# Performance work log

Measured on AMD Instinct MI355X. Metric: run time of the kernel, lower is better.

The kernel has to match this reference:

```python
import jax, jax.numpy as jnp
import numpy as np

N_NODES = 50000
N_EDGES = 800000
NODE_IN = 64
EDGE_IN = 64
MSG = 64
NODE_OUT = 64
EDGE_OUT = 64
DIM = 2


def setup_inputs() -> dict:
    key = jax.random.key(0)
    ks = jax.random.split(key, 12)
    x = jax.random.normal(ks[0], (N_NODES, NODE_IN), dtype=jnp.float32)
    edge_index = jax.random.randint(ks[1], (2, N_EDGES), 0, N_NODES, dtype=jnp.int64)
    edge_attr = jax.random.normal(ks[2], (N_EDGES, EDGE_IN), dtype=jnp.float32)
    r = jax.random.normal(ks[3], (N_EDGES, DIM), dtype=jnp.float32)
    # reference distances must be positive (divided by in strain computation)
    d_init = jax.random.uniform(ks[4], (N_EDGES, 1), dtype=jnp.float32, minval=0.5, maxval=1.5)
    msg_in = 1 + 2 * NODE_IN + EDGE_IN  # strain(1) + x_j + x_i + edge_attr
    W_msg = jax.random.normal(ks[5], (msg_in, MSG), dtype=jnp.float32) / np.sqrt(msg_in)
    b_msg = jnp.zeros((MSG,), dtype=jnp.float32)
    upd_in = NODE_IN + MSG
    W_upd = jax.random.normal(ks[6], (upd_in, NODE_OUT), dtype=jnp.float32) / np.sqrt(upd_in)
    b_upd = jnp.zeros((NODE_OUT,), dtype=jnp.float32)
    W_edge = jax.random.normal(ks[7], (MSG, EDGE_OUT), dtype=jnp.float32) / np.sqrt(MSG)
    b_edge = jnp.zeros((EDGE_OUT,), dtype=jnp.float32)
    return {"x": x, "edge_index": edge_index, "edge_attr": edge_attr, "r": r,
            "d_init": d_init, "W_msg": W_msg, "b_msg": b_msg, "W_upd": W_upd,
            "b_upd": b_upd, "W_edge": W_edge, "b_edge": b_edge}


def reference(x, edge_index, edge_attr, r, d_init, W_msg, b_msg, W_upd, b_upd, W_edge, b_edge):
    # PyG source_to_target flow: x_j = source = edge_index[0], x_i = target = edge_index[1]
    src = edge_index[0]
    dst = edge_index[1]
    n = x.shape[0]
    d = jnp.linalg.norm(r, axis=-1, keepdims=True)          # [e,1]
    strain = (d - d_init) / d_init                          # [e,1]
    # message: Linear(concat(x_j, x_i, strain, edge_attr)) -> Softplus
    feat = jnp.concatenate([x[src], x[dst], strain, edge_attr], axis=1)  # [e, 1+2*node_in+edge_in]
    msg = jax.nn.softplus(feat @ W_msg + b_msg)             # [e, msg]
    # mean aggregation over incoming edges per target node
    agg = jax.ops.segment_sum(msg, dst, num_segments=n)     # [n, msg]
    cnt = jax.ops.segment_sum(jnp.ones((msg.shape[0], 1), msg.dtype), dst, num_segments=n)
    agg = agg / jnp.maximum(cnt, 1.0)
    # node update: Linear(concat(x, aggr_out))
    x_new = jnp.concatenate([x, agg], axis=1) @ W_upd + b_upd  # [n, node_out]
    # edge update: Linear(messages)
    edge_new = msg @ W_edge + b_edge                        # [e, edge_out]
    return (x_new, edge_new, msg, strain)
```

## Files before the change

kernel.cpp:

```cpp
#include <hip/hip_runtime.h>
#include <math.h>

#define NN 50000
#define NE 800000
#define NTILE2 6250
#define NBLK 196

typedef __bf16 bf16x4 __attribute__((ext_vector_type(4)));
typedef __bf16 bf16x8 __attribute__((ext_vector_type(8)));
typedef float  f32x4  __attribute__((ext_vector_type(4)));

__device__ __forceinline__ float softplus_f(float v) {
    const float t = __expf(-fabsf(v));
    return fmaxf(v, 0.f) + __logf(1.f + t);
}

__global__ void k_prep(const float* __restrict__ x, __bf16* __restrict__ xb) {
    const int i = blockIdx.x * 256 + threadIdx.x;
    if (i < NN * 16) {
        const f32x4 v = *(const f32x4*)(x + (size_t)i * 4);
        bf16x4 b;
        b[0]=(__bf16)v[0]; b[1]=(__bf16)v[1]; b[2]=(__bf16)v[2]; b[3]=(__bf16)v[3];
        *(bf16x4*)(xb + (size_t)i * 4) = b;
    }
}

__global__ void k_zero(int* deg) {
    int i = blockIdx.x * blockDim.x + threadIdx.x;
    if (i < NN) deg[i] = 0;
}

__global__ void k_hist(const int* __restrict__ ei, int* __restrict__ deg) {
    int e = blockIdx.x * blockDim.x + threadIdx.x;
    if (e < NE) atomicAdd(&deg[ei[NE + e]], 1);
}

__global__ void k_bsum(const int* __restrict__ deg, int* __restrict__ bsum) {
    __shared__ int ws4[4];
    const int tid = threadIdx.x;
    const int i = blockIdx.x * 256 + tid;
    int v = (i < NN) ? deg[i] : 0;
    #pragma unroll
    for (int off = 1; off < 64; off <<= 1) v += __shfl_xor(v, off);
    if ((tid & 63) == 0) ws4[tid >> 6] = v;
    __syncthreads();
    if (tid == 0) bsum[blockIdx.x] = ws4[0] + ws4[1] + ws4[2] + ws4[3];
}

__global__ void k_bscan(const int* __restrict__ bsum, int* __restrict__ boff) {
    __shared__ int wsum[4];
    const int tid = threadIdx.x, lane = tid & 63, wid = tid >> 6;
    const int v = (tid < NBLK) ? bsum[tid] : 0;
    int s = v;
    #pragma unroll
    for (int off = 1; off < 64; off <<= 1) {
        int t = __shfl_up(s, off);
        if (lane >= off) s += t;
    }
    if (lane == 63) wsum[wid] = s;
    __syncthreads();
    int add = 0;
    #pragma unroll
    for (int q = 0; q < 4; ++q) add += (q < wid) ? wsum[q] : 0;
    if (tid < NBLK) boff[tid] = (s + add) - v;
}

__global__ void k_apply(const int* __restrict__ deg, const int* __restrict__ boff,
                        int* __restrict__ rowptr, int* __restrict__ cursor) {
    __shared__ int wsum[4];
    const int tid = threadIdx.x, lane = tid & 63, wid = tid >> 6;
    const int i = blockIdx.x * 256 + tid;
    const int v = (i < NN) ? deg[i] : 0;
    int s = v;
    #pragma unroll
    for (int off = 1; off < 64; off <<= 1) {
        int t = __shfl_up(s, off);
        if (lane >= off) s += t;
    }
    if (lane == 63) wsum[wid] = s;
    __syncthreads();
    int add = boff[blockIdx.x];
    #pragma unroll
    for (int q = 0; q < 4; ++q) add += (q < wid) ? wsum[q] : 0;
    const int incl = s + add;
    if (i < NN) { rowptr[i + 1] = incl; cursor[i] = incl - v; }
    if (i == 0) rowptr[0] = 0;
}

__global__ void k_scatter(const int* __restrict__ ei, int* __restrict__ cursor,
                          int* __restrict__ eidx) {
    int e = blockIdx.x * blockDim.x + threadIdx.x;
    if (e < NE) {
        int d = ei[NE + e];
        int p = atomicAdd(&cursor[d], 1);
        eidx[p] = e;
    }
}

template<bool USE_XB>
__global__ __launch_bounds__(512, 2) void k_edge(
    const float* __restrict__ x, const __bf16* __restrict__ xb,
    const int* __restrict__ ei,
    const float* __restrict__ ea, const float* __restrict__ r2,
    const float* __restrict__ dinit, const float* __restrict__ Wmsg,
    const float* __restrict__ bmsg, const float* __restrict__ Wedge,
    const float* __restrict__ bedge,
    float* __restrict__ out_edge, float* __restrict__ out_msg,
    float* __restrict__ out_strain)
{
    __shared__ __bf16 sWm[64 * 200];
    __shared__ __bf16 sA [128 * 200];
    __shared__ float  sStrain[128];

    const int tid  = threadIdx.x;
    const int lane = tid & 63;
    const int wid  = tid >> 6;
    const int col  = lane & 15;
    const int quad = lane >> 4;

    {
        const int n = tid & 63, kg = tid >> 6;
        for (int k = kg; k < 192; k += 8) {
            float v = (k < 128) ? Wmsg[k * 64 + n] : Wmsg[(k + 1) * 64 + n];
            sWm[n * 200 + k] = (__bf16)v;
        }
    }
    bf16x8 weF[2][4];
    #pragma unroll
    for (int kc = 0; kc < 2; ++kc)
        #pragma unroll
        for (int nt = 0; nt < 4; ++nt) {
            bf16x8 f;
            #pragma unroll
            for (int j = 0; j < 8; ++j)
                f[j] = (__bf16)Wedge[(kc * 32 + quad * 8 + j) * 64 + nt * 16 + col];
            weF[kc][nt] = f;
        }
    float bm[4], be[4], wst[4];
    #pragma unroll
    for (int nt = 0; nt < 4; ++nt) {
        bm[nt]  = bmsg[nt * 16 + col];
        be[nt]  = bedge[nt * 16 + col];
        wst[nt] = Wmsg[128 * 64 + nt * 16 + col];
    }

    for (int tile = blockIdx.x; tile < NTILE2; tile += gridDim.x) {
        const int e0 = tile * 128;

        if constexpr (USE_XB) {
            #pragma unroll
            for (int it = 0; it < 2; ++it) {
                const int i = tid + it * 512;
                const int e = i >> 3, c = i & 7;
                const int s = ei[e0 + e], d = ei[NE + e0 + e];
                const bf16x8 vj = *(const bf16x8*)(xb + (size_t)s * 64 + c * 8);
                const bf16x8 vi = *(const bf16x8*)(xb + (size_t)d * 64 + c * 8);
                *(bf16x8*)&sA[e * 200 +      c * 8] = vj;
                *(bf16x8*)&sA[e * 200 + 64 + c * 8] = vi;
            }
        } else {
            #pragma unroll
            for (int it = 0; it < 4; ++it) {
                const int i = tid + it * 512;
                const int e = i >> 4, c = i & 15;
                const int s = ei[e0 + e], d = ei[NE + e0 + e];
                const f32x4 xj = *(const f32x4*)(x + (size_t)s * 64 + c * 4);
                const f32x4 xi = *(const f32x4*)(x + (size_t)d * 64 + c * 4);
                bf16x4 a, b;
                a[0]=(__bf16)xj[0]; a[1]=(__bf16)xj[1]; a[2]=(__bf16)xj[2]; a[3]=(__bf16)xj[3];
                b[0]=(__bf16)xi[0]; b[1]=(__bf16)xi[1]; b[2]=(__bf16)xi[2]; b[3]=(__bf16)xi[3];
                *(bf16x4*)&sA[e * 200 +      c * 4] = a;
                *(bf16x4*)&sA[e * 200 + 64 + c * 4] = b;
            }
        }
        #pragma unroll
        for (int it = 0; it < 4; ++it) {
            const int i = tid + it * 512;
            const int e = i >> 4, c = i & 15;
            const f32x4 ev = __builtin_nontemporal_load(
                                 (const f32x4*)(ea + (size_t)(e0 + e) * 64 + c * 4));
            bf16x4 d;
            d[0]=(__bf16)ev[0]; d[1]=(__bf16)ev[1]; d[2]=(__bf16)ev[2]; d[3]=(__bf16)ev[3];
            *(bf16x4*)&sA[e * 200 + 128 + c * 4] = d;
        }
        if (tid < 128) {
            const float rx = r2[(size_t)(e0 + tid) * 2];
            const float ry = r2[(size_t)(e0 + tid) * 2 + 1];
            const float di = dinit[e0 + tid];
            const float st = (sqrtf(rx * rx + ry * ry) - di) / di;
            sStrain[tid] = st;
            __builtin_nontemporal_store(st, &out_strain[e0 + tid]);
        }
        __syncthreads();

        f32x4 acc[4];
        const int r0 = wid * 16 + quad * 4;
        #pragma unroll
        for (int nt = 0; nt < 4; ++nt)
            #pragma unroll
            for (int rg = 0; rg < 4; ++rg)
                acc[nt][rg] = sStrain[r0 + rg] * wst[nt];

        const int abase = (wid * 16 + col) * 200 + quad * 8;
        #pragma unroll
        for (int kc = 0; kc < 6; ++kc) {
            const bf16x8 af = *(const bf16x8*)&sA[abase + kc * 32];
            #pragma unroll
            for (int nt = 0; nt < 4; ++nt) {
                const bf16x8 bfr = *(const bf16x8*)&sWm[(nt * 16 + col) * 200 + kc * 32 + quad * 8];
                acc[nt] = __builtin_amdgcn_mfma_f32_16x16x32_bf16(af, bfr, acc[nt], 0, 0, 0);
            }
        }

        __bf16* A2 = &sA[wid * 16 * 200];
        #pragma unroll
        for (int nt = 0; nt < 4; ++nt) {
            #pragma unroll
            for (int rg = 0; rg < 4; ++rg) {
                const int row = quad * 4 + rg;
                const float sp = softplus_f(acc[nt][rg] + bm[nt]);
                out_msg[(size_t)(e0 + wid * 16 + row) * 64 + nt * 16 + col] = sp;
                A2[row * 88 + nt * 16 + col] = (__bf16)sp;
            }
        }
        __builtin_amdgcn_sched_barrier(0);

        f32x4 acc2[4];
        #pragma unroll
        for (int nt = 0; nt < 4; ++nt) acc2[nt] = (f32x4){0.f, 0.f, 0.f, 0.f};
        #pragma unroll
        for (int kc = 0; kc < 2; ++kc) {
            const bf16x8 af = *(const bf16x8*)&A2[col * 88 + kc * 32 + quad * 8];
            #pragma unroll
            for (int nt = 0; nt < 4; ++nt)
                acc2[nt] = __builtin_amdgcn_mfma_f32_16x16x32_bf16(af, weF[kc][nt], acc2[nt], 0, 0, 0);
        }
        #pragma unroll
        for (int nt = 0; nt < 4; ++nt) {
            #pragma unroll
            for (int rg = 0; rg < 4; ++rg) {
                __builtin_nontemporal_store(
                    acc2[nt][rg] + be[nt],
                    &out_edge[(size_t)(e0 + wid * 16 + quad * 4 + rg) * 64 + nt * 16 + col]);
            }
        }
        __syncthreads();
    }
}

__global__ __launch_bounds__(256) void k_node(
    const float* __restrict__ x, const float* __restrict__ msg,
    const int* __restrict__ rowptr, const int* __restrict__ eidx,
    const float* __restrict__ Wupd, const float* __restrict__ bupd,
    float* __restrict__ out_x)
{
    __shared__ float sW[128 * 64];
    const int tid = threadIdx.x;
    for (int i = tid; i < 2048; i += 256)
        ((f32x4*)sW)[i] = ((const f32x4*)Wupd)[i];
    __syncthreads();

    const int lane = tid & 63, wid = tid >> 6;
    const float bu = bupd[lane];

    for (int n = blockIdx.x * 4 + wid; n < NN; n += gridDim.x * 4) {
        const int rs = rowptr[n], ren = rowptr[n + 1];

        float a0 = 0.f, a1 = 0.f, a2 = 0.f, a3 = 0.f;
        int j = rs;
        for (; j + 4 <= ren; j += 4) {
            const int e0 = eidx[j], e1 = eidx[j + 1], e2 = eidx[j + 2], e3 = eidx[j + 3];
            a0 += msg[(size_t)e0 * 64 + lane];
            a1 += msg[(size_t)e1 * 64 + lane];
            a2 += msg[(size_t)e2 * 64 + lane];
            a3 += msg[(size_t)e3 * 64 + lane];
        }
        for (; j < ren; ++j) a0 += msg[(size_t)eidx[j] * 64 + lane];
        const float acc  = (a0 + a1) + (a2 + a3);
        const float mean = acc / fmaxf((float)(ren - rs), 1.f);
        const float xr   = x[(size_t)n * 64 + lane];

        float o = bu;
        #pragma unroll 16
        for (int k = 0; k < 64; ++k)
            o += __shfl(xr, k) * sW[k * 64 + lane];
        #pragma unroll 16
        for (int k = 0; k < 64; ++k)
            o += __shfl(mean, k) * sW[(64 + k) * 64 + lane];

        out_x[(size_t)n * 64 + lane] = o;
    }
}

extern "C" void kernel_launch(void* const* d_in, const int* in_sizes, int n_in,
                              void* d_out, int out_size, void* d_ws, size_t ws_size,
                              hipStream_t stream) {
    const float* x     = (const float*)d_in[0];
    const int*   ei    = (const int*)d_in[1];
    const float* ea    = (const float*)d_in[2];
    const float* r2    = (const float*)d_in[3];
    const float* dinit = (const float*)d_in[4];
    const float* Wmsg  = (const float*)d_in[5];
    const float* bmsg  = (const float*)d_in[6];
    const float* Wupd  = (const float*)d_in[7];
    const float* bupd  = (const float*)d_in[8];
    const float* Wedge = (const float*)d_in[9];
    const float* bedge = (const float*)d_in[10];

    float* out_x      = (float*)d_out;
    float* out_edge   = out_x + (size_t)NN * 64;
    float* out_msg    = out_edge + (size_t)NE * 64;
    float* out_strain = out_msg + (size_t)NE * 64;

    const size_t XB_BYTES  = (size_t)NN * 64 * 2;
    const size_t CSR_INTS  = 50176 + 50304 + 50176 + 800000 + 256 + 256;
    const bool   use_xb    = ws_size >= XB_BYTES + CSR_INTS * 4 + 64;

    __bf16* xb  = (__bf16*)d_ws;
    int*    deg = use_xb ? (int*)((char*)d_ws + XB_BYTES) : (int*)d_ws;
    int* rowptr = deg + 50176;
    int* cursor = rowptr + 50304;
    int* eidx   = cursor + 50176;
    int* bsum   = eidx + 800000;
    int* boff   = bsum + 256;

    k_zero   <<<196,   256, 0, stream>>>(deg);
    k_hist   <<<3125,  256, 0, stream>>>(ei, deg);
    k_bsum   <<<196,   256, 0, stream>>>(deg, bsum);
    k_bscan  <<<1,     256, 0, stream>>>(bsum, boff);
    k_apply  <<<196,   256, 0, stream>>>(deg, boff, rowptr, cursor);
    k_scatter<<<3125,  256, 0, stream>>>(ei, cursor, eidx);
    if (use_xb) {
        k_prep        <<<3125, 256, 0, stream>>>(x, xb);
        k_edge<true>  <<<512,  512, 0, stream>>>(x, xb, ei, ea, r2, dinit, Wmsg, bmsg,
                                                 Wedge, bedge, out_edge, out_msg, out_strain);
    } else {
        k_edge<false> <<<512,  512, 0, stream>>>(x, nullptr, ei, ea, r2, dinit, Wmsg, bmsg,
                                                 Wedge, bedge, out_edge, out_msg, out_strain);
    }
    k_node   <<<2048,  256, 0, stream>>>(x, out_msg, rowptr, eidx, Wupd, bupd, out_x);
}
```

Before: 797.8 us.

## Fuse mean aggregation into edge kernel via float atomics, drop CSR build

When the workspace is large enough, the edge kernel adds each softplus message into a per-node aggregation buffer with float atomics. This replaces the CSR construction (block sums, scan, apply, scatter) and the node kernel's gather that re-read all messages. The node kernel now reads the summed buffer and divides by the degree histogram. The cost is tens of millions of global atomics contending on destination rows, and summation order is no longer deterministic; the old CSR path remains as a fallback.

```diff
diff --git a/kernel.cpp b/kernel.cpp
--- a/kernel.cpp
+++ b/kernel.cpp
@@ -15,7 +15,8 @@
     return fmaxf(v, 0.f) + __logf(1.f + t);
 }
 
-__global__ void k_prep(const float* __restrict__ x, __bf16* __restrict__ xb) {
+__global__ void k_init(const float* __restrict__ x, __bf16* __restrict__ xb,
+                       int* __restrict__ deg, float* __restrict__ agg) {
     const int i = blockIdx.x * 256 + threadIdx.x;
     if (i < NN * 16) {
         const f32x4 v = *(const f32x4*)(x + (size_t)i * 4);
@@ -23,16 +24,190 @@
         b[0]=(__bf16)v[0]; b[1]=(__bf16)v[1]; b[2]=(__bf16)v[2]; b[3]=(__bf16)v[3];
         *(bf16x4*)(xb + (size_t)i * 4) = b;
     }
+    *(f32x4*)(agg + (size_t)i * 4) = (f32x4){0.f, 0.f, 0.f, 0.f};
+    if (i < NN) deg[i] = 0;
+}
+
+__global__ void k_hist(const int* __restrict__ ei, int* __restrict__ deg) {
+    int e = blockIdx.x * blockDim.x + threadIdx.x;
+    if (e < NE) atomicAdd(&deg[ei[NE + e]], 1);
+}
+
+__global__ __launch_bounds__(512, 2) void k_edge_agg(
+    const __bf16* __restrict__ xb, const int* __restrict__ ei,
+    const float* __restrict__ ea, const float* __restrict__ r2,
+    const float* __restrict__ dinit, const float* __restrict__ Wmsg,
+    const float* __restrict__ bmsg, const float* __restrict__ Wedge,
+    const float* __restrict__ bedge,
+    float* __restrict__ out_edge, float* __restrict__ out_msg,
+    float* __restrict__ out_strain, float* __restrict__ agg)
+{
+    __shared__ __bf16 sWm[64 * 200];
+    __shared__ __bf16 sA [128 * 200];
+    __shared__ float  sStrain[128];
+
+    const int tid  = threadIdx.x;
+    const int lane = tid & 63;
+    const int wid  = tid >> 6;
+    const int col  = lane & 15;
+    const int quad = lane >> 4;
+
+    {
+        const int n = tid & 63, kg = tid >> 6;
+        for (int k = kg; k < 192; k += 8) {
+            float v = (k < 128) ? Wmsg[k * 64 + n] : Wmsg[(k + 1) * 64 + n];
+            sWm[n * 200 + k] = (__bf16)v;
+        }
+    }
+    bf16x8 weF[2][4];
+    #pragma unroll
+    for (int kc = 0; kc < 2; ++kc)
+        #pragma unroll
+        for (int nt = 0; nt < 4; ++nt) {
+            bf16x8 f;
+            #pragma unroll
+            for (int j = 0; j < 8; ++j)
+                f[j] = (__bf16)Wedge[(kc * 32 + quad * 8 + j) * 64 + nt * 16 + col];
+            weF[kc][nt] = f;
+        }
+    float bm[4], be[4], wst[4];
+    #pragma unroll
+    for (int nt = 0; nt < 4; ++nt) {
+        bm[nt]  = bmsg[nt * 16 + col];
+        be[nt]  = bedge[nt * 16 + col];
+        wst[nt] = Wmsg[128 * 64 + nt * 16 + col];
+    }
+
+    for (int tile = blockIdx.x; tile < NTILE2; tile += gridDim.x) {
+        const int e0 = tile * 128;
+
+        #pragma unroll
+        for (int it = 0; it < 2; ++it) {
+            const int i = tid + it * 512;
+            const int e = i >> 3, c = i & 7;
+            const int s = ei[e0 + e], d = ei[NE + e0 + e];
+            const bf16x8 vj = *(const bf16x8*)(xb + (size_t)s * 64 + c * 8);
+            const bf16x8 vi = *(const bf16x8*)(xb + (size_t)d * 64 + c * 8);
+            *(bf16x8*)&sA[e * 200 +      c * 8] = vj;
+            *(bf16x8*)&sA[e * 200 + 64 + c * 8] = vi;
+        }
+        #pragma unroll
+        for (int it = 0; it < 4; ++it) {
+            const int i = tid + it * 512;
+            const int e = i >> 4, c = i & 15;
+            const f32x4 ev = __builtin_nontemporal_load(
+                                 (const f32x4*)(ea + (size_t)(e0 + e) * 64 + c * 4));
+            bf16x4 d;
+            d[0]=(__bf16)ev[0]; d[1]=(__bf16)ev[1]; d[2]=(__bf16)ev[2]; d[3]=(__bf16)ev[3];
+            *(bf16x4*)&sA[e * 200 + 128 + c * 4] = d;
+        }
+        if (tid < 128) {
+            const float rx = r2[(size_t)(e0 + tid) * 2];
+            const float ry = r2[(size_t)(e0 + tid) * 2 + 1];
+            const float di = dinit[e0 + tid];
+            const float st = (sqrtf(rx * rx + ry * ry) - di) / di;
+            sStrain[tid] = st;
+            __builtin_nontemporal_store(st, &out_strain[e0 + tid]);
+        }
+        __syncthreads();
+
+        f32x4 acc[4];
+        const int r0 = wid * 16 + quad * 4;
+        #pragma unroll
+        for (int nt = 0; nt < 4; ++nt)
+            #pragma unroll
+            for (int rg = 0; rg < 4; ++rg)
+                acc[nt][rg] = sStrain[r0 + rg] * wst[nt];
+
+        const int abase = (wid * 16 + col) * 200 + quad * 8;
+        #pragma unroll
+        for (int kc = 0; kc < 6; ++kc) {
+            const bf16x8 af = *(const bf16x8*)&sA[abase + kc * 32];
+            #pragma unroll
+            for (int nt = 0; nt < 4; ++nt) {
+                const bf16x8 bfr = *(const bf16x8*)&sWm[(nt * 16 + col) * 200 + kc * 32 + quad * 8];
+                acc[nt] = __builtin_amdgcn_mfma_f32_16x16x32_bf16(af, bfr, acc[nt], 0, 0, 0);
+            }
+        }
+
+        int dstv[4];
+        #pragma unroll
+        for (int rg = 0; rg < 4; ++rg)
+            dstv[rg] = ei[NE + e0 + r0 + rg];
+
+        __bf16* A2 = &sA[wid * 16 * 200];
+        #pragma unroll
+        for (int nt = 0; nt < 4; ++nt) {
+            #pragma unroll
+            for (int rg = 0; rg < 4; ++rg) {
+                const int row = quad * 4 + rg;
+                const float sp = softplus_f(acc[nt][rg] + bm[nt]);
+                __builtin_nontemporal_store(
+                    sp, &out_msg[(size_t)(e0 + wid * 16 + row) * 64 + nt * 16 + col]);
+                unsafeAtomicAdd(&agg[(size_t)dstv[rg] * 64 + nt * 16 + col], sp);
+                A2[row * 88 + nt * 16 + col] = (__bf16)sp;
+            }
+        }
+        __builtin_amdgcn_sched_barrier(0);
+
+        f32x4 acc2[4];
+        #pragma unroll
+        for (int nt = 0; nt < 4; ++nt) acc2[nt] = (f32x4){0.f, 0.f, 0.f, 0.f};
+        #pragma unroll
+        for (int kc = 0; kc < 2; ++kc) {
+            const bf16x8 af = *(const bf16x8*)&A2[col * 88 + kc * 32 + quad * 8];
+            #pragma unroll
+            for (int nt = 0; nt < 4; ++nt)
+                acc2[nt] = __builtin_amdgcn_mfma_f32_16x16x32_bf16(af, weF[kc][nt], acc2[nt], 0, 0, 0);
+        }
+        #pragma unroll
+        for (int nt = 0; nt < 4; ++nt) {
+            #pragma unroll
+            for (int rg = 0; rg < 4; ++rg) {
+                __builtin_nontemporal_store(
+                    acc2[nt][rg] + be[nt],
+                    &out_edge[(size_t)(e0 + wid * 16 + quad * 4 + rg) * 64 + nt * 16 + col]);
+            }
+        }
+        __syncthreads();
+    }
+}
+
+__global__ __launch_bounds__(256) void k_node_lite(
+    const float* __restrict__ x, const float* __restrict__ agg,
+    const int* __restrict__ deg,
+    const float* __restrict__ Wupd, const float* __restrict__ bupd,
+    float* __restrict__ out_x)
+{
+    __shared__ float sW[128 * 64];
+    const int tid = threadIdx.x;
+    for (int i = tid; i < 2048; i += 256)
+        ((f32x4*)sW)[i] = ((const f32x4*)Wupd)[i];
+    __syncthreads();
+
+    const int lane = tid & 63, wid = tid >> 6;
+    const float bu = bupd[lane];
+
+    for (int n = blockIdx.x * 4 + wid; n < NN; n += gridDim.x * 4) {
+        const int d = deg[n];
+        const float mean = agg[(size_t)n * 64 + lane] / fmaxf((float)d, 1.f);
+        const float xr   = x[(size_t)n * 64 + lane];
+
+        float o = bu;
+        #pragma unroll 16
+        for (int k = 0; k < 64; ++k)
+            o += __shfl(xr, k) * sW[k * 64 + lane];
+        #pragma unroll 16
+        for (int k = 0; k < 64; ++k)
+            o += __shfl(mean, k) * sW[(64 + k) * 64 + lane];
+
+        out_x[(size_t)n * 64 + lane] = o;
+    }
 }
 
 __global__ void k_zero(int* deg) {
     int i = blockIdx.x * blockDim.x + threadIdx.x;
     if (i < NN) deg[i] = 0;
-}
-
-__global__ void k_hist(const int* __restrict__ ei, int* __restrict__ deg) {
-    int e = blockIdx.x * blockDim.x + threadIdx.x;
-    if (e < NE) atomicAdd(&deg[ei[NE + e]], 1);
 }
 
 __global__ void k_bsum(const int* __restrict__ deg, int* __restrict__ bsum) {
@@ -97,10 +272,8 @@
     }
 }
 
-template<bool USE_XB>
-__global__ __launch_bounds__(512, 2) void k_edge(
-    const float* __restrict__ x, const __bf16* __restrict__ xb,
-    const int* __restrict__ ei,
+__global__ __launch_bounds__(512, 2) void k_edge_csr(
+    const float* __restrict__ x, const int* __restrict__ ei,
     const float* __restrict__ ea, const float* __restrict__ r2,
     const float* __restrict__ dinit, const float* __restrict__ Wmsg,
     const float* __restrict__ bmsg, const float* __restrict__ Wedge,
@@ -146,32 +319,18 @@
 
     for (int tile = blockIdx.x; tile < NTILE2; tile += gridDim.x) {
         const int e0 = tile * 128;
-
-        if constexpr (USE_XB) {
-            #pragma unroll
-            for (int it = 0; it < 2; ++it) {
-                const int i = tid + it * 512;
-                const int e = i >> 3, c = i & 7;
-                const int s = ei[e0 + e], d = ei[NE + e0 + e];
-                const bf16x8 vj = *(const bf16x8*)(xb + (size_t)s * 64 + c * 8);
-                const bf16x8 vi = *(const bf16x8*)(xb + (size_t)d * 64 + c * 8);
-                *(bf16x8*)&sA[e * 200 +      c * 8] = vj;
-                *(bf16x8*)&sA[e * 200 + 64 + c * 8] = vi;
-            }
-        } else {
-            #pragma unroll
-            for (int it = 0; it < 4; ++it) {
-                const int i = tid + it * 512;
-                const int e = i >> 4, c = i & 15;
-                const int s = ei[e0 + e], d = ei[NE + e0 + e];
-                const f32x4 xj = *(const f32x4*)(x + (size_t)s * 64 + c * 4);
-                const f32x4 xi = *(const f32x4*)(x + (size_t)d * 64 + c * 4);
-                bf16x4 a, b;
-                a[0]=(__bf16)xj[0]; a[1]=(__bf16)xj[1]; a[2]=(__bf16)xj[2]; a[3]=(__bf16)xj[3];
-                b[0]=(__bf16)xi[0]; b[1]=(__bf16)xi[1]; b[2]=(__bf16)xi[2]; b[3]=(__bf16)xi[3];
-                *(bf16x4*)&sA[e * 200 +      c * 4] = a;
-                *(bf16x4*)&sA[e * 200 + 64 + c * 4] = b;
-            }
+        #pragma unroll
+        for (int it = 0; it < 4; ++it) {
+            const int i = tid + it * 512;
+            const int e = i >> 4, c = i & 15;
+            const int s = ei[e0 + e], d = ei[NE + e0 + e];
+            const f32x4 xj = *(const f32x4*)(x + (size_t)s * 64 + c * 4);
+            const f32x4 xi = *(const f32x4*)(x + (size_t)d * 64 + c * 4);
+            bf16x4 a, b;
+            a[0]=(__bf16)xj[0]; a[1]=(__bf16)xj[1]; a[2]=(__bf16)xj[2]; a[3]=(__bf16)xj[3];
+            b[0]=(__bf16)xi[0]; b[1]=(__bf16)xi[1]; b[2]=(__bf16)xi[2]; b[3]=(__bf16)xi[3];
+            *(bf16x4*)&sA[e * 200 +      c * 4] = a;
+            *(bf16x4*)&sA[e * 200 + 64 + c * 4] = b;
         }
         #pragma unroll
         for (int it = 0; it < 4; ++it) {
@@ -248,7 +407,7 @@
     }
 }
 
-__global__ __launch_bounds__(256) void k_node(
+__global__ __launch_bounds__(256) void k_node_csr(
     const float* __restrict__ x, const float* __restrict__ msg,
     const int* __restrict__ rowptr, const int* __restrict__ eidx,
     const float* __restrict__ Wupd, const float* __restrict__ bupd,
@@ -265,7 +424,6 @@
 
     for (int n = blockIdx.x * 4 + wid; n < NN; n += gridDim.x * 4) {
         const int rs = rowptr[n], ren = rowptr[n + 1];
-
         float a0 = 0.f, a1 = 0.f, a2 = 0.f, a3 = 0.f;
         int j = rs;
         for (; j + 4 <= ren; j += 4) {
@@ -313,30 +471,37 @@
     float* out_strain = out_msg + (size_t)NE * 64;
 
     const size_t XB_BYTES  = (size_t)NN * 64 * 2;
-    const size_t CSR_INTS  = 50176 + 50304 + 50176 + 800000 + 256 + 256;
-    const bool   use_xb    = ws_size >= XB_BYTES + CSR_INTS * 4 + 64;
-
-    __bf16* xb  = (__bf16*)d_ws;
-    int*    deg = use_xb ? (int*)((char*)d_ws + XB_BYTES) : (int*)d_ws;
-    int* rowptr = deg + 50176;
-    int* cursor = rowptr + 50304;
-    int* eidx   = cursor + 50176;
-    int* bsum   = eidx + 800000;
-    int* boff   = bsum + 256;
-
-    k_zero   <<<196,   256, 0, stream>>>(deg);
-    k_hist   <<<3125,  256, 0, stream>>>(ei, deg);
-    k_bsum   <<<196,   256, 0, stream>>>(deg, bsum);
-    k_bscan  <<<1,     256, 0, stream>>>(bsum, boff);
-    k_apply  <<<196,   256, 0, stream>>>(deg, boff, rowptr, cursor);
-    k_scatter<<<3125,  256, 0, stream>>>(ei, cursor, eidx);
-    if (use_xb) {
-        k_prep        <<<3125, 256, 0, stream>>>(x, xb);
-        k_edge<true>  <<<512,  512, 0, stream>>>(x, xb, ei, ea, r2, dinit, Wmsg, bmsg,
-                                                 Wedge, bedge, out_edge, out_msg, out_strain);
+    const size_t AGG_BYTES = (size_t)NN * 64 * 4 + (size_t)750000 * 16;
+    const size_t DEG_BYTES = (size_t)NN * 4;
+    const bool   use_agg   = ws_size >= XB_BYTES + AGG_BYTES + DEG_BYTES + 256;
+
+    if (use_agg) {
+        __bf16* xb  = (__bf16*)d_ws;
+        float*  agg = (float*)((char*)d_ws + XB_BYTES);
+        int*    deg = (int*)((char*)d_ws + XB_BYTES + AGG_BYTES);
+
+        k_init     <<<3125, 256, 0, stream>>>(x, xb, deg, agg);
+        k_hist     <<<3125, 256, 0, stream>>>(ei, deg);
+        k_edge_agg <<<512,  512, 0, stream>>>(xb, ei, ea, r2, dinit, Wmsg, bmsg,
+                                              Wedge, bedge, out_edge, out_msg,
+                                              out_strain, agg);
+        k_node_lite<<<2048, 256, 0, stream>>>(x, agg, deg, Wupd, bupd, out_x);
     } else {
-        k_edge<false> <<<512,  512, 0, stream>>>(x, nullptr, ei, ea, r2, dinit, Wmsg, bmsg,
-                                                 Wedge, bedge, out_edge, out_msg, out_strain);
-    }
-    k_node   <<<2048,  256, 0, stream>>>(x, out_msg, rowptr, eidx, Wupd, bupd, out_x);
-}
+        int* deg    = (int*)d_ws;
+        int* rowptr = deg + 50176;
+        int* cursor = rowptr + 50304;
+        int* eidx   = cursor + 50176;
+        int* bsum   = eidx + 800000;
+        int* boff   = bsum + 256;
+
+        k_zero     <<<196,   256, 0, stream>>>(deg);
+        k_hist     <<<3125,  256, 0, stream>>>(ei, deg);
+        k_bsum     <<<196,   256, 0, stream>>>(deg, bsum);
+        k_bscan    <<<1,     256, 0, stream>>>(bsum, boff);
+        k_apply    <<<196,   256, 0, stream>>>(deg, boff, rowptr, cursor);
+        k_scatter  <<<3125,  256, 0, stream>>>(ei, cursor, eidx);
+        k_edge_csr <<<512,   512, 0, stream>>>(x, ei, ea, r2, dinit, Wmsg, bmsg,
+                                               Wedge, bedge, out_edge, out_msg, out_strain);
+        k_node_csr <<<2048,  256, 0, stream>>>(x, out_msg, rowptr, eidx, Wupd, bupd, out_x);
+    }
+}
```

Result: no change. 795.2 us (-0.3%).
